# Kernel tuning notes

Measured on AMD Instinct MI355X. Metric: run time of the kernel, lower is better.

## Reference

```python
import jax, jax.numpy as jnp
import numpy as np

N = 4096          # nodes
IN_DIM = 256
OUT_DIM = 128
EDGE_DIM = 64
N_SAMPLE = 128
N_EDGES = 65536   # undirected edges (edge ids 1..N_EDGES; id 0 = no edge)
ALPHA = 0.2       # leaky-relu negative slope


def _glorot(key, shape):
    fan_in, fan_out = shape[0], shape[-1]
    scale = 1.414 * np.sqrt(2.0 / (fan_in + fan_out))
    return jax.random.normal(key, shape, jnp.float32) * scale


def setup_inputs() -> dict:
    rng = np.random.default_rng(0)
    # sample unique undirected edges (i < j); np.unique sorts lexicographically,
    # which matches torch's row-major e_index.nonzero() ordering, so assigning
    # sequential ids 1..n here makes edges == arange(1, n+1) in the update step.
    ii = rng.integers(0, N, size=3 * N_EDGES)
    jj = rng.integers(0, N, size=3 * N_EDGES)
    lo, hi = np.minimum(ii, jj), np.maximum(ii, jj)
    ok = lo < hi
    pairs = np.unique(np.stack([lo[ok], hi[ok]], axis=1), axis=0)[:N_EDGES]
    n = pairs.shape[0]
    ids = np.arange(1, n + 1, dtype=np.int32)
    e_index = np.zeros((N, N), np.int32)
    e_index[pairs[:, 0], pairs[:, 1]] = ids
    e_index[pairs[:, 1], pairs[:, 0]] = ids
    # per-node neighbor sampling with replacement (hoisted from torch forward)
    neigh = np.empty((N, N_SAMPLE), np.int32)
    for v in range(N):
        nz = np.nonzero(e_index[v])[0]
        neigh[v] = v if nz.size == 0 else rng.choice(nz, N_SAMPLE)

    key = jax.random.key(0)
    ks = jax.random.split(key, 8)
    return {
        "features": jax.random.normal(ks[0], (N, IN_DIM), jnp.float32),
        "e_index": jnp.asarray(e_index),
        "neigh": jnp.asarray(neigh),
        "to_update": jnp.asarray(pairs.astype(np.int32)),
        "emb": jax.random.normal(ks[1], (n + 1, EDGE_DIM), jnp.float32),
        "W": _glorot(ks[2], (IN_DIM, OUT_DIM)),
        "W2": _glorot(ks[3], (OUT_DIM, EDGE_DIM)),
        "W3": _glorot(ks[4], (EDGE_DIM, EDGE_DIM)),
        "B": _glorot(ks[5], (1, EDGE_DIM)),
        "a": _glorot(ks[6], (2 * OUT_DIM + EDGE_DIM, 1)),
    }


def reference(features, e_index, neigh, to_update, emb, W, W2, W3, B, a):
    x = features @ W                                        # [N, OUT]
    xn = x[neigh]                                           # [N, S, OUT] gather
    eid = jnp.take_along_axis(e_index, neigh, axis=1)       # [N, S] edge ids
    en = emb[eid]                                           # [N, S, ED] gather
    a_input = jnp.concatenate(
        [jnp.broadcast_to(x[:, None, :], xn.shape), xn, en], axis=2
    )                                                       # [N, S, 2*OUT+ED]
    e = jax.nn.leaky_relu((a_input @ a)[..., 0], ALPHA)     # [N, S]
    att = jax.nn.softmax(e, axis=1)                         # dropout = id (eval)
    h_prime = jnp.einsum('ns,nsd->nd', att, xn)             # [N, OUT]
    output = jax.nn.elu(h_prime + x)
    # edge update: (output[i] + output[j]) @ W2 == matmul(output[pair], W2).sum(1)
    edges = e_index[to_update[:, 0], to_update[:, 1]]       # == 1..n
    v_input = (output[to_update[:, 0]] + output[to_update[:, 1]]) @ W2
    e_input = emb[edges] @ W3
    a_in2 = jnp.concatenate([B, e_input + v_input + B], axis=0)  # [n+1, ED]
    emb_new = jax.nn.relu(a_in2 * emb)
    return output, emb_new
```

## Files before the change

kernel.cpp:

```cpp
#include <hip/hip_runtime.h>
#include <hip/hip_bf16.h>

#define N_NODES 4096
#define IN_DIM  256
#define OUT_DIM 128
#define EDGE_DIM 64
#define N_SAMPLE 128

__device__ __forceinline__ float wsum64(float v) {
#pragma unroll
  for (int off = 32; off; off >>= 1) v += __shfl_xor(v, off, 64);
  return v;
}
__device__ __forceinline__ float wmax64(float v) {
#pragma unroll
  for (int off = 32; off; off >>= 1) v = fmaxf(v, __shfl_xor(v, off, 64));
  return v;
}

__global__ void __launch_bounds__(128) gemm_x_kernel(const float* __restrict__ feat,
                                                     const float* __restrict__ W,
                                                     float* __restrict__ x) {
  const int t  = threadIdx.x;
  const int v0 = blockIdx.x * 8;
  __shared__ float f[8][IN_DIM];
  float* fflat = &f[0][0];
  for (int idx = t; idx < 8 * IN_DIM; idx += 128)
    fflat[idx] = feat[v0 * IN_DIM + idx];
  __syncthreads();
  float acc[8] = {0.f, 0.f, 0.f, 0.f, 0.f, 0.f, 0.f, 0.f};
  for (int i = 0; i < IN_DIM; i += 4) {
    const float w0 = W[(i + 0) * OUT_DIM + t];
    const float w1 = W[(i + 1) * OUT_DIM + t];
    const float w2 = W[(i + 2) * OUT_DIM + t];
    const float w3 = W[(i + 3) * OUT_DIM + t];
#pragma unroll
    for (int r = 0; r < 8; ++r) {
      const float4 fv = *reinterpret_cast<const float4*>(&f[r][i]);
      acc[r] += fv.x * w0 + fv.y * w1 + fv.z * w2 + fv.w * w3;
    }
  }
#pragma unroll
  for (int r = 0; r < 8; ++r) x[(v0 + r) * OUT_DIM + t] = acc[r];
}

__global__ void __launch_bounds__(64) s12_kernel(const float* __restrict__ x,
                                                 const float* __restrict__ a,
                                                 float* __restrict__ s1,
                                                 float* __restrict__ s2) {
  const int v = blockIdx.x, l = threadIdx.x;
  const float x0 = x[v * OUT_DIM + l], x1 = x[v * OUT_DIM + 64 + l];
  float c1 = x0 * a[l] + x1 * a[64 + l];
  float c2 = x0 * a[OUT_DIM + l] + x1 * a[OUT_DIM + 64 + l];
  c1 = wsum64(c1);
  c2 = wsum64(c2);
  if (l == 0) { s1[v] = c1; s2[v] = c2; }
}

__global__ void __launch_bounds__(256) s3_kernel(const float* __restrict__ emb,
                                                 const float* __restrict__ a,
                                                 float* __restrict__ s3, int rows) {
  const int w = threadIdx.x >> 6, l = threadIdx.x & 63;
  const int r = blockIdx.x * 4 + w;
  if (r >= rows) return;
  float c = emb[r * EDGE_DIM + l] * a[2 * OUT_DIM + l];
  c = wsum64(c);
  if (l == 0) s3[r] = c;
}

__global__ void __launch_bounds__(256) attn_kernel(const float* __restrict__ x,
                                                   const float* __restrict__ s1,
                                                   const float* __restrict__ s2,
                                                   const float* __restrict__ s3,
                                                   const int* __restrict__ neigh,
                                                   const int* __restrict__ eidx,
                                                   float* __restrict__ out) {
  const int v = blockIdx.x;
  const int t = threadIdx.x;
  const int w = t >> 6, l = t & 63;
  __shared__ float att[N_SAMPLE];
  __shared__ int   us[N_SAMPLE];
  __shared__ float red[4];
  __shared__ float2 hpart[4][64];

  if (t < N_SAMPLE) {
    const int u = neigh[v * N_SAMPLE + t];
    us[t] = u;
    float e = s1[v] + s2[u] + s3[eidx[v * N_NODES + u]];
    e = e > 0.f ? e : 0.2f * e;
    att[t] = e;
    const float m = wmax64(e);
    if (l == 0) red[w] = m;
  }
  __syncthreads();
  const float m = fmaxf(red[0], red[1]);
  if (t < N_SAMPLE) {
    const float p = __expf(att[t] - m);
    att[t] = p;
    const float s = wsum64(p);
    if (l == 0) red[2 + w] = s;
  }
  __syncthreads();
  const float inv = 1.0f / (red[2] + red[3]);

  float2 h = make_float2(0.f, 0.f);
  const int s0 = w * 32;
#pragma unroll 8
  for (int s = s0; s < s0 + 32; ++s) {
    const float a = att[s];
    const float2 xv = *reinterpret_cast<const float2*>(&x[us[s] * OUT_DIM + 2 * l]);
    h.x += a * xv.x;
    h.y += a * xv.y;
  }
  hpart[w][l] = h;
  __syncthreads();

  if (t < 64) {
    float2 H = hpart[0][t];
    const float2 p1 = hpart[1][t], p2 = hpart[2][t], p3 = hpart[3][t];
    H.x += p1.x + p2.x + p3.x;
    H.y += p1.y + p2.y + p3.y;
    const float2 xs = *reinterpret_cast<const float2*>(&x[v * OUT_DIM + 2 * t]);
    float ox = H.x * inv + xs.x;
    float oy = H.y * inv + xs.y;
    ox = ox > 0.f ? ox : expm1f(ox);
    oy = oy > 0.f ? oy : expm1f(oy);
    float2 r = make_float2(ox, oy);
    *reinterpret_cast<float2*>(&out[v * OUT_DIM + 2 * t]) = r;
  }
}

__global__ void __launch_bounds__(256) y_kernel(const float* __restrict__ out,
                                                const float* __restrict__ W2,
                                                float* __restrict__ Y) {
  const int t  = threadIdx.x;
  const int r0 = blockIdx.x * 16;
  __shared__ float o[16][132];
  for (int idx = t; idx < 16 * OUT_DIM; idx += 256)
    o[idx >> 7][idx & 127] = out[r0 * OUT_DIM + idx];
  __syncthreads();
  const int r  = t >> 4;
  const int c0 = (t & 15) * 4;
  float4 acc = make_float4(0.f, 0.f, 0.f, 0.f);
  for (int k = 0; k < OUT_DIM; k += 4) {
#pragma unroll
    for (int kk = 0; kk < 4; ++kk) {
      const float av = o[r][k + kk];
      const float4 w = *reinterpret_cast<const float4*>(&W2[(k + kk) * EDGE_DIM + c0]);
      acc.x += av * w.x; acc.y += av * w.y; acc.z += av * w.z; acc.w += av * w.w;
    }
  }
  *reinterpret_cast<float4*>(&Y[(r0 + r) * EDGE_DIM + c0]) = acc;
}

#define TE 64
__global__ void __launch_bounds__(256) edge_fused_kernel(const float* __restrict__ Y,
                                                         const float* __restrict__ emb,
                                                         const int* __restrict__ eidx,
                                                         const int* __restrict__ tu,
                                                         const float* __restrict__ W3,
                                                         const float* __restrict__ Bv,
                                                         float* __restrict__ emb_new, int n) {
  const int t  = threadIdx.x;
  const int k0 = blockIdx.x * TE;
  __shared__ float Ain[TE][68];
  __shared__ int   tus[2 * TE];

  if (t < 2 * TE) {
    const int idx = 2 * k0 + t;
    tus[t] = (idx < 2 * n) ? tu[idx] : 0;
  }
  {
    const int e  = t >> 2, q = t & 3;
    const int ke = k0 + e;
    if (ke < n) {
      const int i = tu[2 * ke], j = tu[2 * ke + 1];
      const int id = eidx[i * N_NODES + j];
#pragma unroll
      for (int kk = 0; kk < 16; kk += 4) {
        const int k = q * 16 + kk;
        *reinterpret_cast<float4*>(&Ain[e][k]) =
            *reinterpret_cast<const float4*>(&emb[id * EDGE_DIM + k]);
      }
    }
  }
  __syncthreads();

  const int e0 = (t >> 4) * 4;
  const int c0 = (t & 15) * 4;
  const float4 b4 = *reinterpret_cast<const float4*>(&Bv[c0]);
  float4 acc[4];
#pragma unroll
  for (int m = 0; m < 4; ++m) acc[m] = b4;

#pragma unroll 4
  for (int k = 0; k < EDGE_DIM; k += 4) {
    float4 a[4];
#pragma unroll
    for (int m = 0; m < 4; ++m) a[m] = *reinterpret_cast<const float4*>(&Ain[e0 + m][k]);
#pragma unroll
    for (int kk = 0; kk < 4; ++kk) {
      const float4 w = *reinterpret_cast<const float4*>(&W3[(k + kk) * EDGE_DIM + c0]);
#pragma unroll
      for (int m = 0; m < 4; ++m) {
        const float av = reinterpret_cast<const float*>(&a[m])[kk];
        acc[m].x += av * w.x; acc[m].y += av * w.y; acc[m].z += av * w.z; acc[m].w += av * w.w;
      }
    }
  }

#pragma unroll
  for (int m = 0; m < 4; ++m) {
    const int ke = k0 + e0 + m;
    if (ke < n) {
      const int i = tus[2 * (e0 + m)], j = tus[2 * (e0 + m) + 1];
      const float4 yi = *reinterpret_cast<const float4*>(&Y[i * EDGE_DIM + c0]);
      const float4 yj = *reinterpret_cast<const float4*>(&Y[j * EDGE_DIM + c0]);
      const float4 ek = *reinterpret_cast<const float4*>(&emb[(ke + 1) * EDGE_DIM + c0]);
      float4 r;
      r.x = fmaxf((acc[m].x + yi.x + yj.x) * ek.x, 0.f);
      r.y = fmaxf((acc[m].y + yi.y + yj.y) * ek.y, 0.f);
      r.z = fmaxf((acc[m].z + yi.z + yj.z) * ek.z, 0.f);
      r.w = fmaxf((acc[m].w + yi.w + yj.w) * ek.w, 0.f);
      *reinterpret_cast<float4*>(&emb_new[(ke + 1) * EDGE_DIM + c0]) = r;
    }
  }
  if (blockIdx.x == 0 && t < 16) {
    const int cc = t * 4;
    const float4 b0 = *reinterpret_cast<const float4*>(&Bv[cc]);
    const float4 e0v = *reinterpret_cast<const float4*>(&emb[cc]);
    float4 r;
    r.x = fmaxf(b0.x * e0v.x, 0.f);
    r.y = fmaxf(b0.y * e0v.y, 0.f);
    r.z = fmaxf(b0.z * e0v.z, 0.f);
    r.w = fmaxf(b0.w * e0v.w, 0.f);
    *reinterpret_cast<float4*>(&emb_new[cc]) = r;
  }
}

extern "C" void kernel_launch(void* const* d_in, const int* in_sizes, int n_in,
                              void* d_out, int out_size, void* d_ws, size_t ws_size,
                              hipStream_t stream) {
  const float* feat  = (const float*)d_in[0];
  const int*   eidx  = (const int*)d_in[1];
  const int*   neigh = (const int*)d_in[2];
  const int*   tu    = (const int*)d_in[3];
  const float* emb   = (const float*)d_in[4];
  const float* W     = (const float*)d_in[5];
  const float* W2    = (const float*)d_in[6];
  const float* W3    = (const float*)d_in[7];
  const float* Bv    = (const float*)d_in[8];
  const float* a     = (const float*)d_in[9];
  const int n    = in_sizes[3] / 2;
  const int rows = in_sizes[4] / EDGE_DIM;

  float* x  = (float*)d_ws;
  float* s1 = x + N_NODES * OUT_DIM;
  float* s2 = s1 + N_NODES;
  float* s3 = s2 + N_NODES;
  float* Y  = s3 + ((rows + 3) & ~3);

  float* out_nodes = (float*)d_out;
  float* emb_new   = out_nodes + N_NODES * OUT_DIM;

  hipLaunchKernelGGL(gemm_x_kernel, dim3(N_NODES / 8), dim3(128), 0, stream, feat, W, x);
  hipLaunchKernelGGL(s12_kernel, dim3(N_NODES), dim3(64), 0, stream, x, a, s1, s2);
  hipLaunchKernelGGL(s3_kernel, dim3((rows + 3) / 4), dim3(256), 0, stream, emb, a, s3, rows);
  hipLaunchKernelGGL(attn_kernel, dim3(N_NODES), dim3(256), 0, stream,
                     x, s1, s2, s3, neigh, eidx, out_nodes);
  hipLaunchKernelGGL(y_kernel, dim3(N_NODES / 16), dim3(256), 0, stream,
                     out_nodes, W2, Y);
  hipLaunchKernelGGL(edge_fused_kernel, dim3((n + TE - 1) / TE), dim3(256), 0, stream,
                     Y, emb, eidx, tu, W3, Bv, emb_new, n);
}
```

Measured before the change: 199.7 us.

## Fuse score kernels into GEMM and Y projection into attention kernel

The six-kernel pipeline is merged into three. The s1/s2 attention-score dot products are computed in the x GEMM epilogue, and the s3 edge scores are computed by the same blocks with a grid-stride loop. The W2 projection (Y) is computed per node inside the attention kernel from the row held in shared memory. This removes launches and global round-trips for x and out, and the attention gather now uses float4 loads. In exchange, Y is computed one row per block with small per-block work. The Y offset is hardcoded to 65552, which assumes a fixed number of embedding rows.

Result: faster. 181.5 us (-9.1%).

```diff
diff --git a/kernel.cpp b/kernel.cpp
--- a/kernel.cpp
+++ b/kernel.cpp
@@ -17,18 +17,33 @@
   for (int off = 32; off; off >>= 1) v = fmaxf(v, __shfl_xor(v, off, 64));
   return v;
 }
-
-__global__ void __launch_bounds__(128) gemm_x_kernel(const float* __restrict__ feat,
-                                                     const float* __restrict__ W,
-                                                     float* __restrict__ x) {
+__device__ __forceinline__ float sum16(float v) {
+#pragma unroll
+  for (int off = 1; off < 16; off <<= 1) v += __shfl_xor(v, off, 64);
+  return v;
+}
+
+__global__ void __launch_bounds__(128) k1_gemm_s_kernel(const float* __restrict__ feat,
+                                                        const float* __restrict__ W,
+                                                        const float* __restrict__ emb,
+                                                        const float* __restrict__ a,
+                                                        float* __restrict__ x,
+                                                        float* __restrict__ s1,
+                                                        float* __restrict__ s2,
+                                                        float* __restrict__ s3, int rows) {
   const int t  = threadIdx.x;
   const int v0 = blockIdx.x * 8;
   __shared__ float f[8][IN_DIM];
-  float* fflat = &f[0][0];
-  for (int idx = t; idx < 8 * IN_DIM; idx += 128)
-    fflat[idx] = feat[v0 * IN_DIM + idx];
+  __shared__ float redA[16], redB[16];
+  {
+    float4* f4 = reinterpret_cast<float4*>(&f[0][0]);
+    const float4* g4 = reinterpret_cast<const float4*>(&feat[v0 * IN_DIM]);
+#pragma unroll
+    for (int i = 0; i < 4; ++i) f4[t + 128 * i] = g4[t + 128 * i];
+  }
   __syncthreads();
   float acc[8] = {0.f, 0.f, 0.f, 0.f, 0.f, 0.f, 0.f, 0.f};
+#pragma unroll 2
   for (int i = 0; i < IN_DIM; i += 4) {
     const float w0 = W[(i + 0) * OUT_DIM + t];
     const float w1 = W[(i + 1) * OUT_DIM + t];
@@ -40,117 +55,120 @@
       acc[r] += fv.x * w0 + fv.y * w1 + fv.z * w2 + fv.w * w3;
     }
   }
-#pragma unroll
-  for (int r = 0; r < 8; ++r) x[(v0 + r) * OUT_DIM + t] = acc[r];
-}
-
-__global__ void __launch_bounds__(64) s12_kernel(const float* __restrict__ x,
-                                                 const float* __restrict__ a,
-                                                 float* __restrict__ s1,
-                                                 float* __restrict__ s2) {
-  const int v = blockIdx.x, l = threadIdx.x;
-  const float x0 = x[v * OUT_DIM + l], x1 = x[v * OUT_DIM + 64 + l];
-  float c1 = x0 * a[l] + x1 * a[64 + l];
-  float c2 = x0 * a[OUT_DIM + l] + x1 * a[OUT_DIM + 64 + l];
-  c1 = wsum64(c1);
-  c2 = wsum64(c2);
-  if (l == 0) { s1[v] = c1; s2[v] = c2; }
-}
-
-__global__ void __launch_bounds__(256) s3_kernel(const float* __restrict__ emb,
-                                                 const float* __restrict__ a,
-                                                 float* __restrict__ s3, int rows) {
-  const int w = threadIdx.x >> 6, l = threadIdx.x & 63;
-  const int r = blockIdx.x * 4 + w;
-  if (r >= rows) return;
-  float c = emb[r * EDGE_DIM + l] * a[2 * OUT_DIM + l];
-  c = wsum64(c);
-  if (l == 0) s3[r] = c;
-}
-
-__global__ void __launch_bounds__(256) attn_kernel(const float* __restrict__ x,
-                                                   const float* __restrict__ s1,
-                                                   const float* __restrict__ s2,
-                                                   const float* __restrict__ s3,
-                                                   const int* __restrict__ neigh,
-                                                   const int* __restrict__ eidx,
-                                                   float* __restrict__ out) {
+  const int wv = t >> 6;
+  const float a1t = a[t], a2t = a[OUT_DIM + t];
+#pragma unroll
+  for (int r = 0; r < 8; ++r) {
+    x[(v0 + r) * OUT_DIM + t] = acc[r];
+    const float q1 = wsum64(acc[r] * a1t);
+    const float q2 = wsum64(acc[r] * a2t);
+    if ((t & 63) == 0) { redA[wv * 8 + r] = q1; redB[wv * 8 + r] = q2; }
+  }
+  __syncthreads();
+  if (t < 8) {
+    s1[v0 + t] = redA[t] + redA[8 + t];
+    s2[v0 + t] = redB[t] + redB[8 + t];
+  }
+  const int gw  = blockIdx.x * 2 + wv;
+  const int l   = t & 63;
+  const int sub = l >> 4, q = l & 15;
+  const float4 a3q = *reinterpret_cast<const float4*>(&a[2 * OUT_DIM + q * 4]);
+  for (int r0 = gw * 4; r0 < rows; r0 += 4096) {
+    const int r = r0 + sub;
+    float v = 0.f;
+    if (r < rows) {
+      const float4 e4 = *reinterpret_cast<const float4*>(&emb[r * EDGE_DIM + q * 4]);
+      v = e4.x * a3q.x + e4.y * a3q.y + e4.z * a3q.z + e4.w * a3q.w;
+    }
+    v = sum16(v);
+    if (q == 0 && r < rows) s3[r] = v;
+  }
+}
+
+__global__ void __launch_bounds__(256) k2_attn_y_kernel(const float* __restrict__ x,
+                                                        const float* __restrict__ s1,
+                                                        const float* __restrict__ s2,
+                                                        const float* __restrict__ s3,
+                                                        const int* __restrict__ neigh,
+                                                        const int* __restrict__ eidx,
+                                                        const float* __restrict__ W2,
+                                                        float* __restrict__ out,
+                                                        float* __restrict__ Y) {
   const int v = blockIdx.x;
   const int t = threadIdx.x;
   const int w = t >> 6, l = t & 63;
-  __shared__ float att[N_SAMPLE];
-  __shared__ int   us[N_SAMPLE];
-  __shared__ float red[4];
-  __shared__ float2 hpart[4][64];
+  __shared__ float attC[N_SAMPLE];
+  __shared__ int   usC[N_SAMPLE];
+  __shared__ float redC[4];
+  __shared__ float4 hpC[8][32];
+  __shared__ float orow[OUT_DIM];
+  __shared__ float partY[4][EDGE_DIM];
 
   if (t < N_SAMPLE) {
     const int u = neigh[v * N_SAMPLE + t];
-    us[t] = u;
+    usC[t] = u;
     float e = s1[v] + s2[u] + s3[eidx[v * N_NODES + u]];
     e = e > 0.f ? e : 0.2f * e;
-    att[t] = e;
+    attC[t] = e;
     const float m = wmax64(e);
-    if (l == 0) red[w] = m;
-  }
-  __syncthreads();
-  const float m = fmaxf(red[0], red[1]);
+    if (l == 0) redC[w] = m;
+  }
+  __syncthreads();
+  const float m = fmaxf(redC[0], redC[1]);
   if (t < N_SAMPLE) {
-    const float p = __expf(att[t] - m);
-    att[t] = p;
+    const float p = __expf(attC[t] - m);
+    attC[t] = p;
     const float s = wsum64(p);
-    if (l == 0) red[2 + w] = s;
-  }
-  __syncthreads();
-  const float inv = 1.0f / (red[2] + red[3]);
-
-  float2 h = make_float2(0.f, 0.f);
-  const int s0 = w * 32;
+    if (l == 0) redC[2 + w] = s;
+  }
+  __syncthreads();
+  const float inv = 1.0f / (redC[2] + redC[3]);
+
+  {
+    const int half = l >> 5, cq = l & 31;
+    float4 h4 = make_float4(0.f, 0.f, 0.f, 0.f);
+    const int s0 = w * 32;
+#pragma unroll
+    for (int it = 0; it < 16; ++it) {
+      const int s = s0 + 2 * it + half;
+      const float av = attC[s];
+      const float4 xv = *reinterpret_cast<const float4*>(&x[usC[s] * OUT_DIM + cq * 4]);
+      h4.x += av * xv.x; h4.y += av * xv.y; h4.z += av * xv.z; h4.w += av * xv.w;
+    }
+    hpC[w * 2 + half][cq] = h4;
+  }
+  __syncthreads();
+  if (t < 32) {
+    float4 H = make_float4(0.f, 0.f, 0.f, 0.f);
+#pragma unroll
+    for (int p = 0; p < 8; ++p) {
+      const float4 v4 = hpC[p][t];
+      H.x += v4.x; H.y += v4.y; H.z += v4.z; H.w += v4.w;
+    }
+    const float4 xs = *reinterpret_cast<const float4*>(&x[v * OUT_DIM + t * 4]);
+    float o0 = H.x * inv + xs.x, o1 = H.y * inv + xs.y;
+    float o2 = H.z * inv + xs.z, o3 = H.w * inv + xs.w;
+    o0 = o0 > 0.f ? o0 : expm1f(o0);
+    o1 = o1 > 0.f ? o1 : expm1f(o1);
+    o2 = o2 > 0.f ? o2 : expm1f(o2);
+    o3 = o3 > 0.f ? o3 : expm1f(o3);
+    const float4 r = make_float4(o0, o1, o2, o3);
+    *reinterpret_cast<float4*>(&out[v * OUT_DIM + t * 4]) = r;
+    *reinterpret_cast<float4*>(&orow[t * 4]) = r;
+  }
+  __syncthreads();
+
+  {
+    const int c = t & 63, ks = t >> 6;
+    float acc = 0.f;
 #pragma unroll 8
-  for (int s = s0; s < s0 + 32; ++s) {
-    const float a = att[s];
-    const float2 xv = *reinterpret_cast<const float2*>(&x[us[s] * OUT_DIM + 2 * l]);
-    h.x += a * xv.x;
-    h.y += a * xv.y;
-  }
-  hpart[w][l] = h;
-  __syncthreads();
-
-  if (t < 64) {
-    float2 H = hpart[0][t];
-    const float2 p1 = hpart[1][t], p2 = hpart[2][t], p3 = hpart[3][t];
-    H.x += p1.x + p2.x + p3.x;
-    H.y += p1.y + p2.y + p3.y;
-    const float2 xs = *reinterpret_cast<const float2*>(&x[v * OUT_DIM + 2 * t]);
-    float ox = H.x * inv + xs.x;
-    float oy = H.y * inv + xs.y;
-    ox = ox > 0.f ? ox : expm1f(ox);
-    oy = oy > 0.f ? oy : expm1f(oy);
-    float2 r = make_float2(ox, oy);
-    *reinterpret_cast<float2*>(&out[v * OUT_DIM + 2 * t]) = r;
-  }
-}
-
-__global__ void __launch_bounds__(256) y_kernel(const float* __restrict__ out,
-                                                const float* __restrict__ W2,
-                                                float* __restrict__ Y) {
-  const int t  = threadIdx.x;
-  const int r0 = blockIdx.x * 16;
-  __shared__ float o[16][132];
-  for (int idx = t; idx < 16 * OUT_DIM; idx += 256)
-    o[idx >> 7][idx & 127] = out[r0 * OUT_DIM + idx];
-  __syncthreads();
-  const int r  = t >> 4;
-  const int c0 = (t & 15) * 4;
-  float4 acc = make_float4(0.f, 0.f, 0.f, 0.f);
-  for (int k = 0; k < OUT_DIM; k += 4) {
-#pragma unroll
-    for (int kk = 0; kk < 4; ++kk) {
-      const float av = o[r][k + kk];
-      const float4 w = *reinterpret_cast<const float4*>(&W2[(k + kk) * EDGE_DIM + c0]);
-      acc.x += av * w.x; acc.y += av * w.y; acc.z += av * w.z; acc.w += av * w.w;
-    }
-  }
-  *reinterpret_cast<float4*>(&Y[(r0 + r) * EDGE_DIM + c0]) = acc;
+    for (int k = ks * 32; k < ks * 32 + 32; ++k)
+      acc += orow[k] * W2[k * EDGE_DIM + c];
+    partY[ks][c] = acc;
+  }
+  __syncthreads();
+  if (t < EDGE_DIM)
+    Y[v * EDGE_DIM + t] = partY[0][t] + partY[1][t] + partY[2][t] + partY[3][t];
 }
 
 #define TE 64
@@ -195,16 +213,17 @@
 
 #pragma unroll 4
   for (int k = 0; k < EDGE_DIM; k += 4) {
-    float4 a[4];
-#pragma unroll
-    for (int m = 0; m < 4; ++m) a[m] = *reinterpret_cast<const float4*>(&Ain[e0 + m][k]);
+    float4 a4[4];
+#pragma unroll
+    for (int m = 0; m < 4; ++m) a4[m] = *reinterpret_cast<const float4*>(&Ain[e0 + m][k]);
 #pragma unroll
     for (int kk = 0; kk < 4; ++kk) {
-      const float4 w = *reinterpret_cast<const float4*>(&W3[(k + kk) * EDGE_DIM + c0]);
+      const float4 wv = *reinterpret_cast<const float4*>(&W3[(k + kk) * EDGE_DIM + c0]);
 #pragma unroll
       for (int m = 0; m < 4; ++m) {
-        const float av = reinterpret_cast<const float*>(&a[m])[kk];
-        acc[m].x += av * w.x; acc[m].y += av * w.y; acc[m].z += av * w.z; acc[m].w += av * w.w;
+        const float av = reinterpret_cast<const float*>(&a4[m])[kk];
+        acc[m].x += av * wv.x; acc[m].y += av * wv.y;
+        acc[m].z += av * wv.z; acc[m].w += av * wv.w;
       }
     }
   }
@@ -258,18 +277,15 @@
   float* s1 = x + N_NODES * OUT_DIM;
   float* s2 = s1 + N_NODES;
   float* s3 = s2 + N_NODES;
-  float* Y  = s3 + ((rows + 3) & ~3);
+  float* Y  = s3 + 65552;
 
   float* out_nodes = (float*)d_out;
   float* emb_new   = out_nodes + N_NODES * OUT_DIM;
 
-  hipLaunchKernelGGL(gemm_x_kernel, dim3(N_NODES / 8), dim3(128), 0, stream, feat, W, x);
-  hipLaunchKernelGGL(s12_kernel, dim3(N_NODES), dim3(64), 0, stream, x, a, s1, s2);
-  hipLaunchKernelGGL(s3_kernel, dim3((rows + 3) / 4), dim3(256), 0, stream, emb, a, s3, rows);
-  hipLaunchKernelGGL(attn_kernel, dim3(N_NODES), dim3(256), 0, stream,
-                     x, s1, s2, s3, neigh, eidx, out_nodes);
-  hipLaunchKernelGGL(y_kernel, dim3(N_NODES / 16), dim3(256), 0, stream,
-                     out_nodes, W2, Y);
+  hipLaunchKernelGGL(k1_gemm_s_kernel, dim3(N_NODES / 8), dim3(128), 0, stream,
+                     feat, W, emb, a, x, s1, s2, s3, rows);
+  hipLaunchKernelGGL(k2_attn_y_kernel, dim3(N_NODES), dim3(256), 0, stream,
+                     x, s1, s2, s3, neigh, eidx, W2, out_nodes, Y);
   hipLaunchKernelGGL(edge_fused_kernel, dim3((n + TE - 1) / TE), dim3(256), 0, stream,
                      Y, emb, eidx, tu, W3, Bv, emb_new, n);
 }
```
